# Kernel optimization log

Hardware: AMD Instinct MI355X
Metric: run time of the kernel (lower is better)

Reference implementation:

```python
import jax, jax.numpy as jnp
import numpy as np

N = 50000      # nodes
E = 800000     # random edges (self-loops added in reference, per PyG GATConv default)
F_IN = 128
B = 512        # graphs in the batch
NEG_SLOPE = 0.2  # PyG GATConv leaky_relu default


def setup_inputs() -> dict:
    key = jax.random.key(0)
    ks = jax.random.split(key, 12)
    def w(k, shape, fan_in):
        return jax.random.normal(k, shape, jnp.float32) / np.sqrt(fan_in)
    return {
        "x": jax.random.normal(ks[0], (N, F_IN), jnp.float32),
        "edge_index": jax.random.randint(ks[1], (2, E), 0, N, dtype=jnp.int32),
        "batch": jnp.sort(jax.random.randint(ks[2], (N,), 0, B, dtype=jnp.int32)),
        "W1": w(ks[3], (F_IN, 4 * 64), F_IN),
        "a_src1": w(ks[4], (4, 64), 64),
        "a_dst1": w(ks[5], (4, 64), 64),
        "b1": jnp.zeros((4 * 64,), jnp.float32),
        "W2": w(ks[6], (256, 1 * 128), 256),
        "a_src2": w(ks[7], (1, 128), 128),
        "a_dst2": w(ks[8], (1, 128), 128),
        "b2": jnp.zeros((128,), jnp.float32),
        "Wl": w(ks[9], (128, 1), 128),
        "bl": jnp.zeros((1,), jnp.float32),
    }


def gat_layer(x, src, dst, W, a_src, a_dst, b, n):
    H, Fo = a_src.shape
    h = (x @ W).reshape(n, H, Fo)                      # [N,H,Fo]
    alpha_s = jnp.einsum("nhf,hf->nh", h, a_src)       # [N,H]
    alpha_d = jnp.einsum("nhf,hf->nh", h, a_dst)
    e = jax.nn.leaky_relu(alpha_s[src] + alpha_d[dst], NEG_SLOPE)  # [E,H]
    # segment softmax over incoming edges of each dst node
    m = jax.ops.segment_max(e, dst, num_segments=n)    # [N,H]; self-loops => every node hit
    ex = jnp.exp(e - m[dst])
    den = jax.ops.segment_sum(ex, dst, num_segments=n)
    alpha = ex / den[dst]                              # [E,H]
    out = jax.ops.segment_sum(h[src] * alpha[:, :, None], dst, num_segments=n)
    return out.reshape(n, H * Fo) + b


def reference(x, edge_index, batch, W1, a_src1, a_dst1, b1, W2, a_src2, a_dst2, b2, Wl, bl):
    n = x.shape[0]
    loops = jnp.arange(n, dtype=edge_index.dtype)
    src = jnp.concatenate([edge_index[0], loops])
    dst = jnp.concatenate([edge_index[1], loops])
    h = jax.nn.elu(gat_layer(x, src, dst, W1, a_src1, a_dst1, b1, n))
    h = jax.nn.elu(gat_layer(h, src, dst, W2, a_src2, a_dst2, b2, n))
    # dropout omitted (inference)
    sums = jax.ops.segment_sum(h, batch, num_segments=B)
    cnt = jax.ops.segment_sum(jnp.ones((n,), h.dtype), batch, num_segments=B)
    g = sums / jnp.maximum(cnt, 1.0)[:, None]          # global_mean_pool -> [B,128]
    return jax.nn.sigmoid(g @ Wl + bl).reshape(-1)     # [B]
```

## Files before the change

### kernel.cpp

```cpp
#include <hip/hip_runtime.h>
#include <hip/hip_bf16.h>

#define NN 50000
#define EE 800000
#define ETOT 850000
#define BB 512
#define CAP 64
#define NPART 8
#define DPP 6250

typedef __hip_bfloat16 bf16;
typedef __attribute__((ext_vector_type(8))) __bf16 v8bf;
typedef __attribute__((ext_vector_type(4))) float f32x4;

__device__ __forceinline__ float lo2f(unsigned int u) {
    return __uint_as_float(u << 16);
}
__device__ __forceinline__ float hi2f(unsigned int u) {
    return __uint_as_float(u & 0xffff0000u);
}
__device__ __forceinline__ float us2f(unsigned short u) {
    return __uint_as_float(((unsigned int)u) << 16);
}
__device__ __forceinline__ unsigned short f2bfbits(float f) {
    bf16 h = __float2bfloat16(f);
    return *reinterpret_cast<unsigned short*>(&h);
}
__device__ __forceinline__ float lrelu_exp(float ev) {
    ev = ev > 0.f ? ev : 0.2f * ev;
    return __expf(fminf(ev, 80.f));
}

__global__ void k_prep(const float* __restrict__ W1, const float* __restrict__ W2,
                       bf16* __restrict__ wt1, bf16* __restrict__ wt2,
                       int* __restrict__ deg) {
    int idx = blockIdx.x * blockDim.x + threadIdx.x;
    if (idx < 256 * 128) {
        int c = idx >> 7, k = idx & 127;
        wt1[idx] = __float2bfloat16(W1[k * 256 + c]);
    } else {
        int j = idx - 256 * 128;
        int c = j >> 8, k = j & 255;
        wt2[j] = __float2bfloat16(W2[k * 128 + c]);
    }
    if (idx < NN) deg[idx] = 0;
}

__global__ void k_scatter(const int* __restrict__ srcArr, const int* __restrict__ dstArr,
                          int* __restrict__ deg, int* __restrict__ csrc) {
    int part = blockIdx.x & (NPART - 1);
    int e = (blockIdx.x >> 3) * 256 + threadIdx.x;
    if (e >= ETOT) return;
    int d, s;
    if (e < EE) { d = dstArr[e]; s = srcArr[e]; }
    else        { d = e - EE;    s = d; }
    d = min(max(d, 0), NN - 1);
    s = min(max(s, 0), NN - 1);
    int lo = part * DPP;
    if (d >= lo && d < lo + DPP) {
        int p = atomicAdd(&deg[d], 1);
        if (p < CAP) csrc[d * CAP + p] = s;
    }
}

__global__ __launch_bounds__(256, 2)
void k_gemm1(const float* __restrict__ x, const bf16* __restrict__ wt1,
             const float* __restrict__ aw_s, const float* __restrict__ aw_d,
             bf16* __restrict__ h1, float* __restrict__ as1,
             float* __restrict__ ad1) {
    int n0 = blockIdx.x * 32;
    int t = threadIdx.x;
    __shared__ bf16 xs[32 * 136];
    for (int i = 0; i < 4; i++) {
        int idx = t + 256 * i;
        int r = idx >> 5, c4 = idx & 31;
        float4 v = make_float4(0.f, 0.f, 0.f, 0.f);
        if (n0 + r < NN) v = *(const float4*)(x + (size_t)(n0 + r) * 128 + c4 * 4);
        ushort4 o;
        o.x = f2bfbits(v.x); o.y = f2bfbits(v.y);
        o.z = f2bfbits(v.z); o.w = f2bfbits(v.w);
        *(ushort4*)(&xs[r * 136 + c4 * 4]) = o;
    }
    __syncthreads();

    int wv = t >> 6, lane = t & 63;
    int q = lane >> 4, r16 = lane & 15;
    int rowBase = (wv & 1) * 16;
    int colBase = (wv >> 1) * 128;

    f32x4 acc[8];
#pragma unroll
    for (int ct = 0; ct < 8; ct++) acc[ct] = (f32x4){0.f, 0.f, 0.f, 0.f};

#pragma unroll
    for (int kt = 0; kt < 4; kt++) {
        v8bf va = *(const v8bf*)(&xs[(rowBase + r16) * 136 + kt * 32 + q * 8]);
#pragma unroll
        for (int ct = 0; ct < 8; ct++) {
            v8bf vb = *(const v8bf*)(wt1 + (size_t)(colBase + ct * 16 + r16) * 128 + kt * 32 + q * 8);
            acc[ct] = __builtin_amdgcn_mfma_f32_16x16x32_bf16(va, vb, acc[ct], 0, 0, 0);
        }
    }

    float wsv[8], wdv[8];
#pragma unroll
    for (int ct = 0; ct < 8; ct++) {
        int col = colBase + ct * 16 + r16;
        wsv[ct] = aw_s[col];
        wdv[ct] = aw_d[col];
    }

    float ps[4][2], pd[4][2];
#pragma unroll
    for (int reg = 0; reg < 4; reg++) {
        ps[reg][0] = 0.f; ps[reg][1] = 0.f;
        pd[reg][0] = 0.f; pd[reg][1] = 0.f;
    }

#pragma unroll
    for (int reg = 0; reg < 4; reg++) {
        int node = n0 + rowBase + q * 4 + reg;
        bool ok = node < NN;
#pragma unroll
        for (int ct = 0; ct < 8; ct++) {
            float v = acc[ct][reg];
            if (ok) h1[(size_t)node * 256 + colBase + ct * 16 + r16] = __float2bfloat16(v);
            ps[reg][ct >> 2] += v * wsv[ct];
            pd[reg][ct >> 2] += v * wdv[ct];
        }
    }

#pragma unroll
    for (int reg = 0; reg < 4; reg++) {
        int node = n0 + rowBase + q * 4 + reg;
        bool ok = node < NN;
#pragma unroll
        for (int lh = 0; lh < 2; lh++) {
            float a = ps[reg][lh], b = pd[reg][lh];
            for (int mask = 1; mask <= 8; mask <<= 1) {
                a += __shfl_xor(a, mask);
                b += __shfl_xor(b, mask);
            }
            if (r16 == 0 && ok) {
                int head = (wv >> 1) * 2 + lh;
                as1[node * 4 + head] = a;
                ad1[node * 4 + head] = b;
            }
        }
    }
}

__global__ void k_gather1(const int* __restrict__ csrc, const int* __restrict__ deg,
                          const bf16* __restrict__ h1, const float* __restrict__ as1,
                          const float* __restrict__ ad1, const float* __restrict__ b1,
                          bf16* __restrict__ x2) {
    int bid = blockIdx.x;
    int n = bid >> 1, slice = bid & 1;
    int t = threadIdx.x;
    int lh = t >> 5;
    int cnt = min(deg[n], CAP);
    float2 ad = *(const float2*)&ad1[n * 4 + slice * 2];
    __shared__ unsigned int ls[CAP];
    __shared__ float la[CAP * 2];
    const char* h1c = (const char*)h1;
    unsigned int tconst = (unsigned int)(slice * 128 + t * 2) * 2;
    if (t < cnt) {
        int s = csrc[n * CAP + t];
        s = min(max(s, 0), NN - 1);
        ls[t] = (unsigned int)s << 9;
        float2 as = *(const float2*)&as1[s * 4 + slice * 2];
        la[t * 2 + 0] = lrelu_exp(as.x + ad.x);
        la[t * 2 + 1] = lrelu_exp(as.y + ad.y);
    }
    __syncthreads();
    float a0 = 0.f, a1 = 0.f, ssum = 0.f;
    int j = 0;
    for (; j + 3 < cnt; j += 4) {
        unsigned int o0 = ls[j] + tconst, o1 = ls[j + 1] + tconst;
        unsigned int o2 = ls[j + 2] + tconst, o3 = ls[j + 3] + tconst;
        float A0 = la[j * 2 + lh], A1 = la[j * 2 + 2 + lh];
        float A2 = la[j * 2 + 4 + lh], A3 = la[j * 2 + 6 + lh];
        unsigned int u0 = *(const unsigned int*)(h1c + o0);
        unsigned int u1 = *(const unsigned int*)(h1c + o1);
        unsigned int u2 = *(const unsigned int*)(h1c + o2);
        unsigned int u3 = *(const unsigned int*)(h1c + o3);
        ssum += (A0 + A1) + (A2 + A3);
        a0 = fmaf(A0, lo2f(u0), a0); a0 = fmaf(A1, lo2f(u1), a0);
        a0 = fmaf(A2, lo2f(u2), a0); a0 = fmaf(A3, lo2f(u3), a0);
        a1 = fmaf(A0, hi2f(u0), a1); a1 = fmaf(A1, hi2f(u1), a1);
        a1 = fmaf(A2, hi2f(u2), a1); a1 = fmaf(A3, hi2f(u3), a1);
    }
    for (; j < cnt; j++) {
        unsigned int o0 = ls[j] + tconst;
        float A0 = la[j * 2 + lh];
        unsigned int u0 = *(const unsigned int*)(h1c + o0);
        ssum += A0;
        a0 = fmaf(A0, lo2f(u0), a0);
        a1 = fmaf(A0, hi2f(u0), a1);
    }
    float inv = 1.f / fmaxf(ssum, 1e-35f);
    int c = slice * 128 + t * 2;
    float r0 = a0 * inv + b1[c + 0];
    float r1 = a1 * inv + b1[c + 1];
    r0 = r0 > 0.f ? r0 : (__expf(r0) - 1.f);
    r1 = r1 > 0.f ? r1 : (__expf(r1) - 1.f);
    unsigned int packed = (unsigned int)f2bfbits(r0) | ((unsigned int)f2bfbits(r1) << 16);
    *(unsigned int*)((unsigned short*)x2 + (size_t)n * 256 + c) = packed;
}

__global__ __launch_bounds__(256, 2)
void k_gemm2(const bf16* __restrict__ x2, const bf16* __restrict__ wt2,
             const float* __restrict__ aw_s, const float* __restrict__ aw_d,
             bf16* __restrict__ h2, float* __restrict__ as2,
             float* __restrict__ ad2) {
    int n0 = blockIdx.x * 32;
    int t = threadIdx.x;
    __shared__ bf16 xs[32 * 264];
    __shared__ float psPart[32][2];
    __shared__ float pdPart[32][2];
    for (int i = 0; i < 4; i++) {
        int idx = t + 256 * i;
        int r = idx >> 5, c8 = idx & 31;
        uint4 v;
        if (n0 + r < NN) v = *(const uint4*)(x2 + (size_t)(n0 + r) * 256 + c8 * 8);
        else             v = make_uint4(0, 0, 0, 0);
        *(uint4*)(&xs[r * 264 + c8 * 8]) = v;
    }
    __syncthreads();

    int wv = t >> 6, lane = t & 63;
    int q = lane >> 4, r16 = lane & 15;
    int rowBase = (wv & 1) * 16;
    int colBase = (wv >> 1) * 64;

    f32x4 acc[4];
#pragma unroll
    for (int ct = 0; ct < 4; ct++) acc[ct] = (f32x4){0.f, 0.f, 0.f, 0.f};

#pragma unroll
    for (int kt = 0; kt < 8; kt++) {
        v8bf va = *(const v8bf*)(&xs[(rowBase + r16) * 264 + kt * 32 + q * 8]);
#pragma unroll
        for (int ct = 0; ct < 4; ct++) {
            v8bf vb = *(const v8bf*)(wt2 + (size_t)(colBase + ct * 16 + r16) * 256 + kt * 32 + q * 8);
            acc[ct] = __builtin_amdgcn_mfma_f32_16x16x32_bf16(va, vb, acc[ct], 0, 0, 0);
        }
    }

    float wsv[4], wdv[4];
#pragma unroll
    for (int ct = 0; ct < 4; ct++) {
        int col = colBase + ct * 16 + r16;
        wsv[ct] = aw_s[col];
        wdv[ct] = aw_d[col];
    }

#pragma unroll
    for (int reg = 0; reg < 4; reg++) {
        int node = n0 + rowBase + q * 4 + reg;
        bool ok = node < NN;
        float ps = 0.f, pd = 0.f;
#pragma unroll
        for (int ct = 0; ct < 4; ct++) {
            float v = acc[ct][reg];
            if (ok) h2[(size_t)node * 128 + colBase + ct * 16 + r16] = __float2bfloat16(v);
            ps += v * wsv[ct];
            pd += v * wdv[ct];
        }
        for (int mask = 1; mask <= 8; mask <<= 1) {
            ps += __shfl_xor(ps, mask);
            pd += __shfl_xor(pd, mask);
        }
        if (r16 == 0) {
            int li = rowBase + q * 4 + reg;
            psPart[li][wv >> 1] = ps;
            pdPart[li][wv >> 1] = pd;
        }
    }
    __syncthreads();
    if (t < 32) {
        int node = n0 + t;
        if (node < NN) {
            as2[node] = psPart[t][0] + psPart[t][1];
            ad2[node] = pdPart[t][0] + pdPart[t][1];
        }
    }
}

__global__ void k_gather2(const int* __restrict__ csrc, const int* __restrict__ deg,
                          const bf16* __restrict__ h2, const float* __restrict__ as2,
                          const float* __restrict__ ad2, const float* __restrict__ b2,
                          bf16* __restrict__ hf) {
    int n = blockIdx.x;
    int t = threadIdx.x;
    int cnt = min(deg[n], CAP);
    float adn = ad2[n];
    __shared__ unsigned int ls[CAP];
    __shared__ float la[CAP];
    const char* h2c = (const char*)h2;
    unsigned int tconst = (unsigned int)t * 4;
    if (t < cnt) {
        int s = csrc[n * CAP + t];
        s = min(max(s, 0), NN - 1);
        ls[t] = (unsigned int)s << 8;
        la[t] = lrelu_exp(as2[s] + adn);
    }
    __syncthreads();
    float a0 = 0.f, a1 = 0.f, ssum = 0.f;
    int j = 0;
    for (; j + 3 < cnt; j += 4) {
        unsigned int o0 = ls[j] + tconst, o1 = ls[j + 1] + tconst;
        unsigned int o2 = ls[j + 2] + tconst, o3 = ls[j + 3] + tconst;
        float A0 = la[j], A1 = la[j + 1], A2 = la[j + 2], A3 = la[j + 3];
        unsigned int u0 = *(const unsigned int*)(h2c + o0);
        unsigned int u1 = *(const unsigned int*)(h2c + o1);
        unsigned int u2 = *(const unsigned int*)(h2c + o2);
        unsigned int u3 = *(const unsigned int*)(h2c + o3);
        ssum += (A0 + A1) + (A2 + A3);
        a0 = fmaf(A0, lo2f(u0), a0); a0 = fmaf(A1, lo2f(u1), a0);
        a0 = fmaf(A2, lo2f(u2), a0); a0 = fmaf(A3, lo2f(u3), a0);
        a1 = fmaf(A0, hi2f(u0), a1); a1 = fmaf(A1, hi2f(u1), a1);
        a1 = fmaf(A2, hi2f(u2), a1); a1 = fmaf(A3, hi2f(u3), a1);
    }
    for (; j < cnt; j++) {
        unsigned int o0 = ls[j] + tconst;
        float A0 = la[j];
        unsigned int u0 = *(const unsigned int*)(h2c + o0);
        ssum += A0;
        a0 = fmaf(A0, lo2f(u0), a0);
        a1 = fmaf(A0, hi2f(u0), a1);
    }
    float inv = 1.f / fmaxf(ssum, 1e-35f);
    int c = t * 2;
    float r0 = a0 * inv + b2[c + 0];
    float r1 = a1 * inv + b2[c + 1];
    r0 = r0 > 0.f ? r0 : (__expf(r0) - 1.f);
    r1 = r1 > 0.f ? r1 : (__expf(r1) - 1.f);
    unsigned int packed = (unsigned int)f2bfbits(r0) | ((unsigned int)f2bfbits(r1) << 16);
    *(unsigned int*)((unsigned short*)hf + (size_t)n * 128 + c) = packed;
}

__global__ void k_pool(const bf16* __restrict__ hf, const int* __restrict__ batch,
                       const float* __restrict__ Wl, const float* __restrict__ bl,
                       float* __restrict__ out) {
    int b = blockIdx.x;
    int t = threadIdx.x;
    int lo = 0, hi = NN;
    while (lo < hi) { int m = (lo + hi) >> 1; if (batch[m] < b) lo = m + 1; else hi = m; }
    int start = lo;
    int lo2 = start, hi2 = NN;
    while (lo2 < hi2) { int m = (lo2 + hi2) >> 1; if (batch[m] < b + 1) lo2 = m + 1; else hi2 = m; }
    int end = lo2;
    const unsigned short* hu = (const unsigned short*)hf;
    float sum = 0.f;
    for (int n = start; n < end; n++) sum += us2f(hu[(size_t)n * 128 + t]);
    int c = end - start;
    float g = sum / (float)(c > 0 ? c : 1);
    float p = g * Wl[t];
    for (int o = 32; o > 0; o >>= 1) p += __shfl_down(p, o);
    __shared__ float red[2];
    if ((t & 63) == 0) red[t >> 6] = p;
    __syncthreads();
    if (t == 0) {
        float acc = red[0] + red[1] + bl[0];
        out[b] = 1.f / (1.f + __expf(-acc));
    }
}

extern "C" void kernel_launch(void* const* d_in, const int* in_sizes, int n_in,
                              void* d_out, int out_size, void* d_ws, size_t ws_size,
                              hipStream_t stream) {
    const float* x = (const float*)d_in[0];
    const int* ei = (const int*)d_in[1];
    const int* batch = (const int*)d_in[2];
    const float* W1 = (const float*)d_in[3];
    const float* aw_s1 = (const float*)d_in[4];
    const float* aw_d1 = (const float*)d_in[5];
    const float* b1 = (const float*)d_in[6];
    const float* W2 = (const float*)d_in[7];
    const float* aw_s2 = (const float*)d_in[8];
    const float* aw_d2 = (const float*)d_in[9];
    const float* b2 = (const float*)d_in[10];
    const float* Wl = (const float*)d_in[11];
    const float* bl = (const float*)d_in[12];
    const int* srcArr = ei;
    const int* dstArr = ei + EE;

    char* w = (char*)d_ws;
    size_t off = 0;
    auto alloc = [&](size_t bytes) -> void* {
        void* p = (void*)(w + off);
        off = (off + bytes + 255) & ~(size_t)255;
        return p;
    };
    bf16* bufA = (bf16*)alloc((size_t)NN * 256 * 2);
    bf16* bufB = (bf16*)alloc((size_t)NN * 256 * 2);
    int* csrc = (int*)alloc((size_t)NN * CAP * 4);
    float* as1 = (float*)alloc((size_t)NN * 4 * 4);
    float* ad1 = (float*)alloc((size_t)NN * 4 * 4);
    float* as2 = (float*)alloc((size_t)NN * 4);
    float* ad2 = (float*)alloc((size_t)NN * 4);
    int* deg = (int*)alloc((size_t)NN * 4);
    bf16* wt1 = (bf16*)alloc((size_t)256 * 128 * 2);
    bf16* wt2 = (bf16*)alloc((size_t)128 * 256 * 2);
    (void)ws_size;

    k_prep<<<256, 256, 0, stream>>>(W1, W2, wt1, wt2, deg);
    int chunks = (ETOT + 255) / 256;
    k_scatter<<<chunks * NPART, 256, 0, stream>>>(srcArr, dstArr, deg, csrc);

    bf16* h1 = bufA;
    bf16* x2 = bufB;
    k_gemm1<<<(NN + 31) / 32, 256, 0, stream>>>(x, wt1, aw_s1, aw_d1, h1, as1, ad1);
    k_gather1<<<NN * 2, 64, 0, stream>>>(csrc, deg, h1, as1, ad1, b1, x2);

    bf16* h2 = bufA;
    k_gemm2<<<(NN + 31) / 32, 256, 0, stream>>>(x2, wt2, aw_s2, aw_d2, h2, as2, ad2);

    bf16* hf = bufB;
    k_gather2<<<NN, 64, 0, stream>>>(csrc, deg, h2, as2, ad2, b2, hf);

    k_pool<<<BB, 128, 0, stream>>>(hf, batch, Wl, bl, (float*)d_out);
}
```

Before: 333.5 us.

## Merge gather blocks into 128-thread blocks and vectorize LDS neighbor reads

Gather1 now runs one 128-thread block per node covering both 128-column slices, so the neighbor list and attention logits for all four heads are computed once instead of twice. Gather2 packs two nodes per 128-thread block, which halves the block count. Both kernels read offsets and weights from LDS as uint4/float4 vectors and carry launch bounds of (128, 8). The aims are less duplicated index and score work and lower per-block launch overhead. The cost is that wave pairs in gather2 now share a barrier, so a low-degree node waits on its partner.

```diff
diff --git a/kernel.cpp b/kernel.cpp
--- a/kernel.cpp
+++ b/kernel.cpp
@@ -150,56 +150,61 @@
     }
 }
 
-__global__ void k_gather1(const int* __restrict__ csrc, const int* __restrict__ deg,
-                          const bf16* __restrict__ h1, const float* __restrict__ as1,
-                          const float* __restrict__ ad1, const float* __restrict__ b1,
-                          bf16* __restrict__ x2) {
-    int bid = blockIdx.x;
-    int n = bid >> 1, slice = bid & 1;
+__global__ __launch_bounds__(128, 8)
+void k_gather1(const int* __restrict__ csrc, const int* __restrict__ deg,
+               const bf16* __restrict__ h1, const float* __restrict__ as1,
+               const float* __restrict__ ad1, const float* __restrict__ b1,
+               bf16* __restrict__ x2) {
+    int n = blockIdx.x;
     int t = threadIdx.x;
-    int lh = t >> 5;
+    int slice = t >> 6;
+    int u = t & 63;
+    int lhG = slice * 2 + (u >> 5);
     int cnt = min(deg[n], CAP);
-    float2 ad = *(const float2*)&ad1[n * 4 + slice * 2];
     __shared__ unsigned int ls[CAP];
-    __shared__ float la[CAP * 2];
+    __shared__ float la[4 * CAP];
     const char* h1c = (const char*)h1;
-    unsigned int tconst = (unsigned int)(slice * 128 + t * 2) * 2;
+    unsigned int tconst = (unsigned int)(slice * 128 + u * 2) * 2;
     if (t < cnt) {
         int s = csrc[n * CAP + t];
         s = min(max(s, 0), NN - 1);
         ls[t] = (unsigned int)s << 9;
-        float2 as = *(const float2*)&as1[s * 4 + slice * 2];
-        la[t * 2 + 0] = lrelu_exp(as.x + ad.x);
-        la[t * 2 + 1] = lrelu_exp(as.y + ad.y);
-    }
-    __syncthreads();
+        float4 as = *(const float4*)&as1[s * 4];
+        float4 ad = *(const float4*)&ad1[n * 4];
+        la[0 * CAP + t] = lrelu_exp(as.x + ad.x);
+        la[1 * CAP + t] = lrelu_exp(as.y + ad.y);
+        la[2 * CAP + t] = lrelu_exp(as.z + ad.z);
+        la[3 * CAP + t] = lrelu_exp(as.w + ad.w);
+    }
+    __syncthreads();
+    const float* lah = &la[lhG * CAP];
     float a0 = 0.f, a1 = 0.f, ssum = 0.f;
     int j = 0;
     for (; j + 3 < cnt; j += 4) {
-        unsigned int o0 = ls[j] + tconst, o1 = ls[j + 1] + tconst;
-        unsigned int o2 = ls[j + 2] + tconst, o3 = ls[j + 3] + tconst;
-        float A0 = la[j * 2 + lh], A1 = la[j * 2 + 2 + lh];
-        float A2 = la[j * 2 + 4 + lh], A3 = la[j * 2 + 6 + lh];
+        uint4 ov = *(const uint4*)&ls[j];
+        float4 Av = *(const float4*)&lah[j];
+        unsigned int o0 = ov.x + tconst, o1 = ov.y + tconst;
+        unsigned int o2 = ov.z + tconst, o3 = ov.w + tconst;
         unsigned int u0 = *(const unsigned int*)(h1c + o0);
         unsigned int u1 = *(const unsigned int*)(h1c + o1);
         unsigned int u2 = *(const unsigned int*)(h1c + o2);
         unsigned int u3 = *(const unsigned int*)(h1c + o3);
-        ssum += (A0 + A1) + (A2 + A3);
-        a0 = fmaf(A0, lo2f(u0), a0); a0 = fmaf(A1, lo2f(u1), a0);
-        a0 = fmaf(A2, lo2f(u2), a0); a0 = fmaf(A3, lo2f(u3), a0);
-        a1 = fmaf(A0, hi2f(u0), a1); a1 = fmaf(A1, hi2f(u1), a1);
-        a1 = fmaf(A2, hi2f(u2), a1); a1 = fmaf(A3, hi2f(u3), a1);
+        ssum += (Av.x + Av.y) + (Av.z + Av.w);
+        a0 = fmaf(Av.x, lo2f(u0), a0); a0 = fmaf(Av.y, lo2f(u1), a0);
+        a0 = fmaf(Av.z, lo2f(u2), a0); a0 = fmaf(Av.w, lo2f(u3), a0);
+        a1 = fmaf(Av.x, hi2f(u0), a1); a1 = fmaf(Av.y, hi2f(u1), a1);
+        a1 = fmaf(Av.z, hi2f(u2), a1); a1 = fmaf(Av.w, hi2f(u3), a1);
     }
     for (; j < cnt; j++) {
         unsigned int o0 = ls[j] + tconst;
-        float A0 = la[j * 2 + lh];
+        float A0 = lah[j];
         unsigned int u0 = *(const unsigned int*)(h1c + o0);
         ssum += A0;
         a0 = fmaf(A0, lo2f(u0), a0);
         a1 = fmaf(A0, hi2f(u0), a1);
     }
     float inv = 1.f / fmaxf(ssum, 1e-35f);
-    int c = slice * 128 + t * 2;
+    int c = slice * 128 + u * 2;
     float r0 = a0 * inv + b1[c + 0];
     float r1 = a1 * inv + b1[c + 1];
     r0 = r0 > 0.f ? r0 : (__expf(r0) - 1.f);
@@ -287,44 +292,47 @@
     }
 }
 
-__global__ void k_gather2(const int* __restrict__ csrc, const int* __restrict__ deg,
-                          const bf16* __restrict__ h2, const float* __restrict__ as2,
-                          const float* __restrict__ ad2, const float* __restrict__ b2,
-                          bf16* __restrict__ hf) {
-    int n = blockIdx.x;
-    int t = threadIdx.x;
+__global__ __launch_bounds__(128, 8)
+void k_gather2(const int* __restrict__ csrc, const int* __restrict__ deg,
+               const bf16* __restrict__ h2, const float* __restrict__ as2,
+               const float* __restrict__ ad2, const float* __restrict__ b2,
+               bf16* __restrict__ hf) {
+    int wv = threadIdx.x >> 6;
+    int n = blockIdx.x * 2 + wv;
+    int t = threadIdx.x & 63;
     int cnt = min(deg[n], CAP);
     float adn = ad2[n];
-    __shared__ unsigned int ls[CAP];
-    __shared__ float la[CAP];
+    __shared__ unsigned int ls[2][CAP];
+    __shared__ float la[2][CAP];
     const char* h2c = (const char*)h2;
     unsigned int tconst = (unsigned int)t * 4;
     if (t < cnt) {
         int s = csrc[n * CAP + t];
         s = min(max(s, 0), NN - 1);
-        ls[t] = (unsigned int)s << 8;
-        la[t] = lrelu_exp(as2[s] + adn);
+        ls[wv][t] = (unsigned int)s << 8;
+        la[wv][t] = lrelu_exp(as2[s] + adn);
     }
     __syncthreads();
     float a0 = 0.f, a1 = 0.f, ssum = 0.f;
     int j = 0;
     for (; j + 3 < cnt; j += 4) {
-        unsigned int o0 = ls[j] + tconst, o1 = ls[j + 1] + tconst;
-        unsigned int o2 = ls[j + 2] + tconst, o3 = ls[j + 3] + tconst;
-        float A0 = la[j], A1 = la[j + 1], A2 = la[j + 2], A3 = la[j + 3];
+        uint4 ov = *(const uint4*)&ls[wv][j];
+        float4 Av = *(const float4*)&la[wv][j];
+        unsigned int o0 = ov.x + tconst, o1 = ov.y + tconst;
+        unsigned int o2 = ov.z + tconst, o3 = ov.w + tconst;
         unsigned int u0 = *(const unsigned int*)(h2c + o0);
         unsigned int u1 = *(const unsigned int*)(h2c + o1);
         unsigned int u2 = *(const unsigned int*)(h2c + o2);
         unsigned int u3 = *(const unsigned int*)(h2c + o3);
-        ssum += (A0 + A1) + (A2 + A3);
-        a0 = fmaf(A0, lo2f(u0), a0); a0 = fmaf(A1, lo2f(u1), a0);
-        a0 = fmaf(A2, lo2f(u2), a0); a0 = fmaf(A3, lo2f(u3), a0);
-        a1 = fmaf(A0, hi2f(u0), a1); a1 = fmaf(A1, hi2f(u1), a1);
-        a1 = fmaf(A2, hi2f(u2), a1); a1 = fmaf(A3, hi2f(u3), a1);
+        ssum += (Av.x + Av.y) + (Av.z + Av.w);
+        a0 = fmaf(Av.x, lo2f(u0), a0); a0 = fmaf(Av.y, lo2f(u1), a0);
+        a0 = fmaf(Av.z, lo2f(u2), a0); a0 = fmaf(Av.w, lo2f(u3), a0);
+        a1 = fmaf(Av.x, hi2f(u0), a1); a1 = fmaf(Av.y, hi2f(u1), a1);
+        a1 = fmaf(Av.z, hi2f(u2), a1); a1 = fmaf(Av.w, hi2f(u3), a1);
     }
     for (; j < cnt; j++) {
-        unsigned int o0 = ls[j] + tconst;
-        float A0 = la[j];
+        unsigned int o0 = ls[wv][j] + tconst;
+        float A0 = la[wv][j];
         unsigned int u0 = *(const unsigned int*)(h2c + o0);
         ssum += A0;
         a0 = fmaf(A0, lo2f(u0), a0);
@@ -412,13 +420,13 @@
     bf16* h1 = bufA;
     bf16* x2 = bufB;
     k_gemm1<<<(NN + 31) / 32, 256, 0, stream>>>(x, wt1, aw_s1, aw_d1, h1, as1, ad1);
-    k_gather1<<<NN * 2, 64, 0, stream>>>(csrc, deg, h1, as1, ad1, b1, x2);
+    k_gather1<<<NN, 128, 0, stream>>>(csrc, deg, h1, as1, ad1, b1, x2);
 
     bf16* h2 = bufA;
     k_gemm2<<<(NN + 31) / 32, 256, 0, stream>>>(x2, wt2, aw_s2, aw_d2, h2, as2, ad2);
 
     bf16* hf = bufB;
-    k_gather2<<<NN, 64, 0, stream>>>(csrc, deg, h2, as2, ad2, b2, hf);
+    k_gather2<<<NN / 2, 128, 0, stream>>>(csrc, deg, h2, as2, ad2, b2, hf);
 
     k_pool<<<BB, 128, 0, stream>>>(hf, batch, Wl, bl, (float*)d_out);
 }
```

New measurement: 336.7 us. No clear change (+1.0%).

## Restructure gather kernels to split edges across lane groups and use 16-bit CSR indices

Applied to the files above, without the earlier changes.

The gather kernels now pack four destination nodes per 256-thread block and split each node's features into column slices. Within a wave, four lane groups each process a strided subset of the edges, and the partial sums are combined with cross-lane shuffles. Each lane fetches 4-byte chunks from 64-byte row segments. CSR source indices are stored as 16-bit values, which halves index traffic, and the clamp on source indices is removed. The goal is to issue more independent gathers per wave with better occupancy and less index bandwidth, at the cost of shuffle reductions and recomputing the attention logits once per slice block.

```diff
diff --git a/kernel.cpp b/kernel.cpp
--- a/kernel.cpp
+++ b/kernel.cpp
@@ -47,7 +47,7 @@
 }
 
 __global__ void k_scatter(const int* __restrict__ srcArr, const int* __restrict__ dstArr,
-                          int* __restrict__ deg, int* __restrict__ csrc) {
+                          int* __restrict__ deg, unsigned short* __restrict__ csrc) {
     int part = blockIdx.x & (NPART - 1);
     int e = (blockIdx.x >> 3) * 256 + threadIdx.x;
     if (e >= ETOT) return;
@@ -59,7 +59,7 @@
     int lo = part * DPP;
     if (d >= lo && d < lo + DPP) {
         int p = atomicAdd(&deg[d], 1);
-        if (p < CAP) csrc[d * CAP + p] = s;
+        if (p < CAP) csrc[d * CAP + p] = (unsigned short)s;
     }
 }
 
@@ -150,62 +150,72 @@
     }
 }
 
-__global__ void k_gather1(const int* __restrict__ csrc, const int* __restrict__ deg,
-                          const bf16* __restrict__ h1, const float* __restrict__ as1,
-                          const float* __restrict__ ad1, const float* __restrict__ b1,
-                          bf16* __restrict__ x2) {
-    int bid = blockIdx.x;
-    int n = bid >> 1, slice = bid & 1;
-    int t = threadIdx.x;
-    int lh = t >> 5;
+__global__ __launch_bounds__(256, 8)
+void k_gather1(const unsigned short* __restrict__ csrc, const int* __restrict__ deg,
+               const bf16* __restrict__ h1, const float* __restrict__ as1,
+               const float* __restrict__ ad1, const float* __restrict__ b1,
+               bf16* __restrict__ x2) {
+    int slice = blockIdx.x & 7;
+    int ng = blockIdx.x >> 3;
+    int wv = threadIdx.x >> 6;
+    int n = ng * 4 + wv;
+    int l = threadIdx.x & 63;
+    int head = slice >> 1;
     int cnt = min(deg[n], CAP);
-    float2 ad = *(const float2*)&ad1[n * 4 + slice * 2];
-    __shared__ unsigned int ls[CAP];
-    __shared__ float la[CAP * 2];
+    __shared__ uint2 lsla[4][CAP];
+    if (l < cnt) {
+        int s = (int)csrc[n * CAP + l];
+        uint2 v;
+        v.x = (unsigned int)s << 9;
+        v.y = __float_as_uint(lrelu_exp(as1[s * 4 + head] + ad1[n * 4 + head]));
+        lsla[wv][l] = v;
+    }
+    __syncthreads();
+    const uint2* lw = lsla[wv];
     const char* h1c = (const char*)h1;
-    unsigned int tconst = (unsigned int)(slice * 128 + t * 2) * 2;
-    if (t < cnt) {
-        int s = csrc[n * CAP + t];
-        s = min(max(s, 0), NN - 1);
-        ls[t] = (unsigned int)s << 9;
-        float2 as = *(const float2*)&as1[s * 4 + slice * 2];
-        la[t * 2 + 0] = lrelu_exp(as.x + ad.x);
-        la[t * 2 + 1] = lrelu_exp(as.y + ad.y);
-    }
-    __syncthreads();
+    int g = l >> 4;
+    int c = l & 15;
+    unsigned int tconst = (unsigned int)(slice * 64 + c * 4);
     float a0 = 0.f, a1 = 0.f, ssum = 0.f;
     int j = 0;
+    for (; j + 7 < cnt; j += 8) {
+        uint2 e0 = lw[j + g];
+        uint2 e1 = lw[j + 4 + g];
+        float A0 = __uint_as_float(e0.y);
+        float A1 = __uint_as_float(e1.y);
+        unsigned int u0 = *(const unsigned int*)(h1c + (e0.x + tconst));
+        unsigned int u1 = *(const unsigned int*)(h1c + (e1.x + tconst));
+        ssum += A0 + A1;
+        a0 = fmaf(A0, lo2f(u0), a0); a1 = fmaf(A0, hi2f(u0), a1);
+        a0 = fmaf(A1, lo2f(u1), a0); a1 = fmaf(A1, hi2f(u1), a1);
+    }
     for (; j + 3 < cnt; j += 4) {
-        unsigned int o0 = ls[j] + tconst, o1 = ls[j + 1] + tconst;
-        unsigned int o2 = ls[j + 2] + tconst, o3 = ls[j + 3] + tconst;
-        float A0 = la[j * 2 + lh], A1 = la[j * 2 + 2 + lh];
-        float A2 = la[j * 2 + 4 + lh], A3 = la[j * 2 + 6 + lh];
-        unsigned int u0 = *(const unsigned int*)(h1c + o0);
-        unsigned int u1 = *(const unsigned int*)(h1c + o1);
-        unsigned int u2 = *(const unsigned int*)(h1c + o2);
-        unsigned int u3 = *(const unsigned int*)(h1c + o3);
-        ssum += (A0 + A1) + (A2 + A3);
-        a0 = fmaf(A0, lo2f(u0), a0); a0 = fmaf(A1, lo2f(u1), a0);
-        a0 = fmaf(A2, lo2f(u2), a0); a0 = fmaf(A3, lo2f(u3), a0);
-        a1 = fmaf(A0, hi2f(u0), a1); a1 = fmaf(A1, hi2f(u1), a1);
-        a1 = fmaf(A2, hi2f(u2), a1); a1 = fmaf(A3, hi2f(u3), a1);
-    }
-    for (; j < cnt; j++) {
-        unsigned int o0 = ls[j] + tconst;
-        float A0 = la[j * 2 + lh];
-        unsigned int u0 = *(const unsigned int*)(h1c + o0);
+        uint2 e0 = lw[j + g];
+        float A0 = __uint_as_float(e0.y);
+        unsigned int u0 = *(const unsigned int*)(h1c + (e0.x + tconst));
         ssum += A0;
-        a0 = fmaf(A0, lo2f(u0), a0);
-        a1 = fmaf(A0, hi2f(u0), a1);
-    }
-    float inv = 1.f / fmaxf(ssum, 1e-35f);
-    int c = slice * 128 + t * 2;
-    float r0 = a0 * inv + b1[c + 0];
-    float r1 = a1 * inv + b1[c + 1];
-    r0 = r0 > 0.f ? r0 : (__expf(r0) - 1.f);
-    r1 = r1 > 0.f ? r1 : (__expf(r1) - 1.f);
-    unsigned int packed = (unsigned int)f2bfbits(r0) | ((unsigned int)f2bfbits(r1) << 16);
-    *(unsigned int*)((unsigned short*)x2 + (size_t)n * 256 + c) = packed;
+        a0 = fmaf(A0, lo2f(u0), a0); a1 = fmaf(A0, hi2f(u0), a1);
+    }
+    if (j + g < cnt) {
+        uint2 e0 = lw[j + g];
+        float A0 = __uint_as_float(e0.y);
+        unsigned int u0 = *(const unsigned int*)(h1c + (e0.x + tconst));
+        ssum += A0;
+        a0 = fmaf(A0, lo2f(u0), a0); a1 = fmaf(A0, hi2f(u0), a1);
+    }
+    a0 += __shfl_xor(a0, 16); a1 += __shfl_xor(a1, 16); ssum += __shfl_xor(ssum, 16);
+    a0 += __shfl_xor(a0, 32); a1 += __shfl_xor(a1, 32); ssum += __shfl_xor(ssum, 32);
+    if (l < 16) {
+        float inv = 1.f / fmaxf(ssum, 1e-35f);
+        int col = slice * 32 + c * 2;
+        float2 bv = *(const float2*)&b1[col];
+        float r0 = a0 * inv + bv.x;
+        float r1 = a1 * inv + bv.y;
+        r0 = r0 > 0.f ? r0 : (__expf(r0) - 1.f);
+        r1 = r1 > 0.f ? r1 : (__expf(r1) - 1.f);
+        unsigned int packed = (unsigned int)f2bfbits(r0) | ((unsigned int)f2bfbits(r1) << 16);
+        *(unsigned int*)((unsigned short*)x2 + (size_t)n * 256 + col) = packed;
+    }
 }
 
 __global__ __launch_bounds__(256, 2)
@@ -287,57 +297,71 @@
     }
 }
 
-__global__ void k_gather2(const int* __restrict__ csrc, const int* __restrict__ deg,
-                          const bf16* __restrict__ h2, const float* __restrict__ as2,
-                          const float* __restrict__ ad2, const float* __restrict__ b2,
-                          bf16* __restrict__ hf) {
-    int n = blockIdx.x;
-    int t = threadIdx.x;
+__global__ __launch_bounds__(256, 8)
+void k_gather2(const unsigned short* __restrict__ csrc, const int* __restrict__ deg,
+               const bf16* __restrict__ h2, const float* __restrict__ as2,
+               const float* __restrict__ ad2, const float* __restrict__ b2,
+               bf16* __restrict__ hf) {
+    int slice = blockIdx.x & 3;
+    int ng = blockIdx.x >> 2;
+    int wv = threadIdx.x >> 6;
+    int n = ng * 4 + wv;
+    int l = threadIdx.x & 63;
     int cnt = min(deg[n], CAP);
-    float adn = ad2[n];
-    __shared__ unsigned int ls[CAP];
-    __shared__ float la[CAP];
+    __shared__ uint2 lsla[4][CAP];
+    if (l < cnt) {
+        int s = (int)csrc[n * CAP + l];
+        uint2 v;
+        v.x = (unsigned int)s << 8;
+        v.y = __float_as_uint(lrelu_exp(as2[s] + ad2[n]));
+        lsla[wv][l] = v;
+    }
+    __syncthreads();
+    const uint2* lw = lsla[wv];
     const char* h2c = (const char*)h2;
-    unsigned int tconst = (unsigned int)t * 4;
-    if (t < cnt) {
-        int s = csrc[n * CAP + t];
-        s = min(max(s, 0), NN - 1);
-        ls[t] = (unsigned int)s << 8;
-        la[t] = lrelu_exp(as2[s] + adn);
-    }
-    __syncthreads();
+    int g = l >> 4;
+    int c = l & 15;
+    unsigned int tconst = (unsigned int)(slice * 64 + c * 4);
     float a0 = 0.f, a1 = 0.f, ssum = 0.f;
     int j = 0;
+    for (; j + 7 < cnt; j += 8) {
+        uint2 e0 = lw[j + g];
+        uint2 e1 = lw[j + 4 + g];
+        float A0 = __uint_as_float(e0.y);
+        float A1 = __uint_as_float(e1.y);
+        unsigned int u0 = *(const unsigned int*)(h2c + (e0.x + tconst));
+        unsigned int u1 = *(const unsigned int*)(h2c + (e1.x + tconst));
+        ssum += A0 + A1;
+        a0 = fmaf(A0, lo2f(u0), a0); a1 = fmaf(A0, hi2f(u0), a1);
+        a0 = fmaf(A1, lo2f(u1), a0); a1 = fmaf(A1, hi2f(u1), a1);
+    }
     for (; j + 3 < cnt; j += 4) {
-        unsigned int o0 = ls[j] + tconst, o1 = ls[j + 1] + tconst;
-        unsigned int o2 = ls[j + 2] + tconst, o3 = ls[j + 3] + tconst;
-        float A0 = la[j], A1 = la[j + 1], A2 = la[j + 2], A3 = la[j + 3];
-        unsigned int u0 = *(const unsigned int*)(h2c + o0);
-        unsigned int u1 = *(const unsigned int*)(h2c + o1);
-        unsigned int u2 = *(const unsigned int*)(h2c + o2);
-        unsigned int u3 = *(const unsigned int*)(h2c + o3);
-        ssum += (A0 + A1) + (A2 + A3);
-        a0 = fmaf(A0, lo2f(u0), a0); a0 = fmaf(A1, lo2f(u1), a0);
-        a0 = fmaf(A2, lo2f(u2), a0); a0 = fmaf(A3, lo2f(u3), a0);
-        a1 = fmaf(A0, hi2f(u0), a1); a1 = fmaf(A1, hi2f(u1), a1);
-        a1 = fmaf(A2, hi2f(u2), a1); a1 = fmaf(A3, hi2f(u3), a1);
-    }
-    for (; j < cnt; j++) {
-        unsigned int o0 = ls[j] + tconst;
-        float A0 = la[j];
-        unsigned int u0 = *(const unsigned int*)(h2c + o0);
+        uint2 e0 = lw[j + g];
+        float A0 = __uint_as_float(e0.y);
+        unsigned int u0 = *(const unsigned int*)(h2c + (e0.x + tconst));
         ssum += A0;
-        a0 = fmaf(A0, lo2f(u0), a0);
-        a1 = fmaf(A0, hi2f(u0), a1);
-    }
-    float inv = 1.f / fmaxf(ssum, 1e-35f);
-    int c = t * 2;
-    float r0 = a0 * inv + b2[c + 0];
-    float r1 = a1 * inv + b2[c + 1];
-    r0 = r0 > 0.f ? r0 : (__expf(r0) - 1.f);
-    r1 = r1 > 0.f ? r1 : (__expf(r1) - 1.f);
-    unsigned int packed = (unsigned int)f2bfbits(r0) | ((unsigned int)f2bfbits(r1) << 16);
-    *(unsigned int*)((unsigned short*)hf + (size_t)n * 128 + c) = packed;
+        a0 = fmaf(A0, lo2f(u0), a0); a1 = fmaf(A0, hi2f(u0), a1);
+    }
+    if (j + g < cnt) {
+        uint2 e0 = lw[j + g];
+        float A0 = __uint_as_float(e0.y);
+        unsigned int u0 = *(const unsigned int*)(h2c + (e0.x + tconst));
+        ssum += A0;
+        a0 = fmaf(A0, lo2f(u0), a0); a1 = fmaf(A0, hi2f(u0), a1);
+    }
+    a0 += __shfl_xor(a0, 16); a1 += __shfl_xor(a1, 16); ssum += __shfl_xor(ssum, 16);
+    a0 += __shfl_xor(a0, 32); a1 += __shfl_xor(a1, 32); ssum += __shfl_xor(ssum, 32);
+    if (l < 16) {
+        float inv = 1.f / fmaxf(ssum, 1e-35f);
+        int col = slice * 32 + c * 2;
+        float2 bv = *(const float2*)&b2[col];
+        float r0 = a0 * inv + bv.x;
+        float r1 = a1 * inv + bv.y;
+        r0 = r0 > 0.f ? r0 : (__expf(r0) - 1.f);
+        r1 = r1 > 0.f ? r1 : (__expf(r1) - 1.f);
+        unsigned int packed = (unsigned int)f2bfbits(r0) | ((unsigned int)f2bfbits(r1) << 16);
+        *(unsigned int*)((unsigned short*)hf + (size_t)n * 128 + col) = packed;
+    }
 }
 
 __global__ void k_pool(const bf16* __restrict__ hf, const int* __restrict__ batch,
@@ -395,7 +419,7 @@
     };
     bf16* bufA = (bf16*)alloc((size_t)NN * 256 * 2);
     bf16* bufB = (bf16*)alloc((size_t)NN * 256 * 2);
-    int* csrc = (int*)alloc((size_t)NN * CAP * 4);
+    unsigned short* csrc = (unsigned short*)alloc((size_t)NN * CAP * 2);
     float* as1 = (float*)alloc((size_t)NN * 4 * 4);
     float* ad1 = (float*)alloc((size_t)NN * 4 * 4);
     float* as2 = (float*)alloc((size_t)NN * 4);
@@ -412,13 +436,13 @@
     bf16* h1 = bufA;
     bf16* x2 = bufB;
     k_gemm1<<<(NN + 31) / 32, 256, 0, stream>>>(x, wt1, aw_s1, aw_d1, h1, as1, ad1);
-    k_gather1<<<NN * 2, 64, 0, stream>>>(csrc, deg, h1, as1, ad1, b1, x2);
+    k_gather1<<<(NN / 4) * 8, 256, 0, stream>>>(csrc, deg, h1, as1, ad1, b1, x2);
 
     bf16* h2 = bufA;
     k_gemm2<<<(NN + 31) / 32, 256, 0, stream>>>(x2, wt2, aw_s2, aw_d2, h2, as2, ad2);
 
     bf16* hf = bufB;
-    k_gather2<<<NN, 64, 0, stream>>>(csrc, deg, h2, as2, ad2, b2, hf);
+    k_gather2<<<(NN / 4) * 4, 256, 0, stream>>>(csrc, deg, h2, as2, ad2, b2, hf);
 
     k_pool<<<BB, 128, 0, stream>>>(hf, batch, Wl, bl, (float*)d_out);
 }
```

Result: slower. 472.9 us (+41.8%).

## Fuse edge scatter with layer-1 GEMM in one launch and store CSR indices as uint16

Applied to the files above, without the earlier changes.

The edge scatter and the first GEMM become one kernel: the first 2048 blocks run a grid-stride scatter and the rest do the GEMM, so the two independent jobs can run side by side and one launch is saved. The CSR source indices are stored as unsigned short instead of int, which halves csrc traffic in both gather kernels and drops their clamps. The risk is that uint16 only holds values up to 65535, which covers the 50000 nodes here. The scatter blocks now inherit the GEMM's shared memory and launch bounds, which could hurt their occupancy.

```diff
diff --git a/kernel.cpp b/kernel.cpp
--- a/kernel.cpp
+++ b/kernel.cpp
@@ -8,6 +8,7 @@
 #define CAP 64
 #define NPART 8
 #define DPP 6250
+#define SCAT_BLKS 2048
 
 typedef __hip_bfloat16 bf16;
 typedef __attribute__((ext_vector_type(8))) __bf16 v8bf;
@@ -46,31 +47,36 @@
     if (idx < NN) deg[idx] = 0;
 }
 
-__global__ void k_scatter(const int* __restrict__ srcArr, const int* __restrict__ dstArr,
-                          int* __restrict__ deg, int* __restrict__ csrc) {
-    int part = blockIdx.x & (NPART - 1);
-    int e = (blockIdx.x >> 3) * 256 + threadIdx.x;
-    if (e >= ETOT) return;
-    int d, s;
-    if (e < EE) { d = dstArr[e]; s = srcArr[e]; }
-    else        { d = e - EE;    s = d; }
-    d = min(max(d, 0), NN - 1);
-    s = min(max(s, 0), NN - 1);
-    int lo = part * DPP;
-    if (d >= lo && d < lo + DPP) {
-        int p = atomicAdd(&deg[d], 1);
-        if (p < CAP) csrc[d * CAP + p] = s;
-    }
-}
-
 __global__ __launch_bounds__(256, 2)
-void k_gemm1(const float* __restrict__ x, const bf16* __restrict__ wt1,
-             const float* __restrict__ aw_s, const float* __restrict__ aw_d,
-             bf16* __restrict__ h1, float* __restrict__ as1,
-             float* __restrict__ ad1) {
-    int n0 = blockIdx.x * 32;
+void k_scatter_gemm1(const int* __restrict__ srcArr, const int* __restrict__ dstArr,
+                     int* __restrict__ deg, unsigned short* __restrict__ csrc,
+                     const float* __restrict__ x, const bf16* __restrict__ wt1,
+                     const float* __restrict__ aw_s, const float* __restrict__ aw_d,
+                     bf16* __restrict__ h1, float* __restrict__ as1,
+                     float* __restrict__ ad1) {
+    __shared__ bf16 xs[32 * 136];
+    if (blockIdx.x < SCAT_BLKS) {
+        int part = blockIdx.x & (NPART - 1);
+        int lo = part * DPP;
+        int t = threadIdx.x;
+        const int STRIDE = (SCAT_BLKS >> 3) * 256;
+        for (int e = (blockIdx.x >> 3) * 256 + t; e < ETOT; e += STRIDE) {
+            int d, s;
+            if (e < EE) { d = dstArr[e]; s = srcArr[e]; }
+            else        { d = e - EE;    s = d; }
+            d = min(max(d, 0), NN - 1);
+            s = min(max(s, 0), NN - 1);
+            if (d >= lo && d < lo + DPP) {
+                int p = atomicAdd(&deg[d], 1);
+                if (p < CAP) csrc[d * CAP + p] = (unsigned short)s;
+            }
+        }
+        return;
+    }
+
+    int bid = blockIdx.x - SCAT_BLKS;
+    int n0 = bid * 32;
     int t = threadIdx.x;
-    __shared__ bf16 xs[32 * 136];
     for (int i = 0; i < 4; i++) {
         int idx = t + 256 * i;
         int r = idx >> 5, c4 = idx & 31;
@@ -150,7 +156,7 @@
     }
 }
 
-__global__ void k_gather1(const int* __restrict__ csrc, const int* __restrict__ deg,
+__global__ void k_gather1(const unsigned short* __restrict__ csrc, const int* __restrict__ deg,
                           const bf16* __restrict__ h1, const float* __restrict__ as1,
                           const float* __restrict__ ad1, const float* __restrict__ b1,
                           bf16* __restrict__ x2) {
@@ -165,8 +171,7 @@
     const char* h1c = (const char*)h1;
     unsigned int tconst = (unsigned int)(slice * 128 + t * 2) * 2;
     if (t < cnt) {
-        int s = csrc[n * CAP + t];
-        s = min(max(s, 0), NN - 1);
+        int s = (int)csrc[n * CAP + t];
         ls[t] = (unsigned int)s << 9;
         float2 as = *(const float2*)&as1[s * 4 + slice * 2];
         la[t * 2 + 0] = lrelu_exp(as.x + ad.x);
@@ -287,7 +292,7 @@
     }
 }
 
-__global__ void k_gather2(const int* __restrict__ csrc, const int* __restrict__ deg,
+__global__ void k_gather2(const unsigned short* __restrict__ csrc, const int* __restrict__ deg,
                           const bf16* __restrict__ h2, const float* __restrict__ as2,
                           const float* __restrict__ ad2, const float* __restrict__ b2,
                           bf16* __restrict__ hf) {
@@ -300,8 +305,7 @@
     const char* h2c = (const char*)h2;
     unsigned int tconst = (unsigned int)t * 4;
     if (t < cnt) {
-        int s = csrc[n * CAP + t];
-        s = min(max(s, 0), NN - 1);
+        int s = (int)csrc[n * CAP + t];
         ls[t] = (unsigned int)s << 8;
         la[t] = lrelu_exp(as2[s] + adn);
     }
@@ -395,7 +399,7 @@
     };
     bf16* bufA = (bf16*)alloc((size_t)NN * 256 * 2);
     bf16* bufB = (bf16*)alloc((size_t)NN * 256 * 2);
-    int* csrc = (int*)alloc((size_t)NN * CAP * 4);
+    unsigned short* csrc = (unsigned short*)alloc((size_t)NN * CAP * 2);
     float* as1 = (float*)alloc((size_t)NN * 4 * 4);
     float* ad1 = (float*)alloc((size_t)NN * 4 * 4);
     float* as2 = (float*)alloc((size_t)NN * 4);
@@ -406,16 +410,17 @@
     (void)ws_size;
 
     k_prep<<<256, 256, 0, stream>>>(W1, W2, wt1, wt2, deg);
-    int chunks = (ETOT + 255) / 256;
-    k_scatter<<<chunks * NPART, 256, 0, stream>>>(srcArr, dstArr, deg, csrc);
 
     bf16* h1 = bufA;
     bf16* x2 = bufB;
-    k_gemm1<<<(NN + 31) / 32, 256, 0, stream>>>(x, wt1, aw_s1, aw_d1, h1, as1, ad1);
+    int gemmBlocks = (NN + 31) / 32;
+    k_scatter_gemm1<<<SCAT_BLKS + gemmBlocks, 256, 0, stream>>>(
+        srcArr, dstArr, deg, csrc, x, wt1, aw_s1, aw_d1, h1, as1, ad1);
+
     k_gather1<<<NN * 2, 64, 0, stream>>>(csrc, deg, h1, as1, ad1, b1, x2);
 
     bf16* h2 = bufA;
-    k_gemm2<<<(NN + 31) / 32, 256, 0, stream>>>(x2, wt2, aw_s2, aw_d2, h2, as2, ad2);
+    k_gemm2<<<gemmBlocks, 256, 0, stream>>>(x2, wt2, aw_s2, aw_d2, h2, as2, ad2);
 
     bf16* hf = bufB;
     k_gather2<<<NN, 64, 0, stream>>>(csrc, deg, h2, as2, ad2, b2, hf);
```

Measured after the change: 329.4 us. About the same (-1.2%).
